# Kernel tuning notes

Measured on AMD Instinct MI355X. Metric: run time of the kernel, lower is better.

The kernel has to match this reference:

```python
import jax, jax.numpy as jnp
import numpy as np

N = 50000
E = 800000
F_IN, F_HID, F_OUT = 128, 128, 64


def setup_inputs() -> dict:
    key = jax.random.key(0)
    ks = jax.random.split(key, 8)
    x = jax.random.normal(ks[0], (N, F_IN), dtype=jnp.float32)
    attn_edge_index = jax.random.randint(ks[1], (2, E), 0, N, dtype=jnp.int64)
    attn_edge_weight = jax.random.uniform(ks[2], (E,), dtype=jnp.float32)
    # GCNConv params (glorot-ish scale); PyG lin has no bias, conv bias added after aggregation
    W1 = jax.random.normal(ks[3], (F_IN, F_HID), dtype=jnp.float32) * (1.0 / np.sqrt(F_IN))
    b1 = jnp.zeros((F_HID,), dtype=jnp.float32)
    W2 = jax.random.normal(ks[4], (F_HID, F_OUT), dtype=jnp.float32) * (1.0 / np.sqrt(F_HID))
    b2 = jnp.zeros((F_OUT,), dtype=jnp.float32)
    return {"x": x, "attn_edge_index": attn_edge_index, "attn_edge_weight": attn_edge_weight,
            "W1": W1, "b1": b1, "W2": W2, "b2": b2}


def _gcn_norm(edge_index, edge_weight, num_nodes):
    # Add self-loops with weight 1 (PyG gcn_norm default)
    loop = jnp.arange(num_nodes, dtype=edge_index.dtype)
    src = jnp.concatenate([edge_index[0], loop])
    dst = jnp.concatenate([edge_index[1], loop])
    w = jnp.concatenate([edge_weight, jnp.ones((num_nodes,), edge_weight.dtype)])
    deg = jax.ops.segment_sum(w, dst, num_segments=num_nodes)  # in-degree weighted
    dinv = jnp.where(deg > 0, jax.lax.rsqrt(deg), 0.0)
    norm = dinv[src] * w * dinv[dst]  # symmetric normalization
    return src, dst, norm


def _gcn_conv(h, src, dst, norm, W, b, num_nodes):
    h = h @ W                                   # [N, Fout] dense transform
    msg = norm[:, None] * h[src]                # [E+N, Fout] gather-multiply
    out = jax.ops.segment_sum(msg, dst, num_segments=num_nodes)  # scatter-add
    return out + b


def reference(x, attn_edge_index, attn_edge_weight, W1, b1, W2, b2):
    num_nodes = x.shape[0]
    src, dst, norm = _gcn_norm(attn_edge_index, attn_edge_weight, num_nodes)
    h = _gcn_conv(x, src, dst, norm, W1, b1, num_nodes)
    h = jax.nn.relu(h)
    # dropout(p=0.5) is identity in eval mode
    h = _gcn_conv(h, src, dst, norm, W2, b2, num_nodes)
    return h
```

## Files before the change

### kernel.cpp

```cpp
#include <hip/hip_runtime.h>
#include <hip/hip_bf16.h>

static constexpr int FIN   = 128;
static constexpr int FHID  = 128;
static constexpr int FOUTC = 64;
static constexpr int CAP   = 48;

typedef short bf16x8 __attribute__((ext_vector_type(8)));
typedef float f32x4 __attribute__((ext_vector_type(4)));

__device__ __forceinline__ float bfbits2f(unsigned short u) {
  union { unsigned i; float f; } c; c.i = ((unsigned)u) << 16; return c.f;
}
__device__ __forceinline__ float wbits2f(unsigned u) {
  union { unsigned i; float f; } c; c.i = u; return c.f;
}
__device__ __forceinline__ unsigned f2wbits(float f) {
  union { float fv; unsigned i; } c; c.fv = f; return c.i;
}
__device__ __forceinline__ void unpack_bf2(unsigned u, float& lo, float& hi) {
  union { unsigned i; float f; } a, b;
  a.i = u << 16;
  b.i = u & 0xffff0000u;
  lo = a.f; hi = b.f;
}
__device__ __forceinline__ unsigned short f2bfbits(float f) {
  union { float fv; unsigned i; } c; c.fv = f;
  unsigned i = c.i;
  unsigned r = i + 0x7FFFu + ((i >> 16) & 1u);
  if ((i & 0x7F800000u) == 0x7F800000u) r = i;
  return (unsigned short)(r >> 16);
}
__device__ __forceinline__ int ld_idx(const void* ei, int is64, long long off) {
  return is64 ? (int)((const long long*)ei)[off] : ((const int*)ei)[off];
}
__device__ __forceinline__ float ld_f(const void* p, int isbf, long long i) {
  return isbf ? bfbits2f(((const unsigned short*)p)[i]) : ((const float*)p)[i];
}

__global__ void setup_kernel(const unsigned short* __restrict__ xb,
                             const unsigned* __restrict__ eiw, int* __restrict__ flags,
                             int* __restrict__ cnt, int n) {
  int i = blockIdx.x * 256 + threadIdx.x;
  if (i < n) cnt[i] = 0;
  if (i == 0) {
    int isbf = 1;
    for (int k = 0; k < 256; ++k) {
      unsigned e = (xb[2 * k] >> 7) & 0xFFu;
      if (e >= 0xC0u) { isbf = 0; break; }
    }
    int is64 = 1;
    for (int k = 0; k < 64; ++k)
      if (eiw[2 * k + 1] != 0u) { is64 = 0; break; }
    flags[0] = isbf;
    flags[1] = is64;
  }
}

__global__ void fill_ell(const void* __restrict__ ei, const void* __restrict__ ew,
                         const int* __restrict__ flg, int* __restrict__ cnt,
                         uint2* __restrict__ ell, int E) {
  int e = blockIdx.x * 256 + threadIdx.x;
  if (e >= E) return;
  int is64 = flg[1];
  int s = ld_idx(ei, is64, e);
  int d = ld_idx(ei, is64, (long long)E + e);
  float w = ld_f(ew, flg[0], e);
  int p = atomicAdd(&cnt[d], 1);
  if (p < CAP) ell[(size_t)d * CAP + p] = make_uint2((unsigned)s, f2wbits(w));
}

__global__ void node_dinv(int* __restrict__ cnt, const uint2* __restrict__ ell,
                          float* __restrict__ dinv, int n) {
  int wid = (blockIdx.x * 256 + threadIdx.x) >> 6;
  int lane = threadIdx.x & 63;
  if (wid >= n) return;
  int c0 = cnt[wid];
  int c = c0 > CAP ? CAP : c0;
  uint2 rec = ell[(size_t)wid * CAP + (lane < CAP ? lane : CAP - 1)];
  float w = (lane < c) ? wbits2f(rec.y) : 0.f;
#pragma unroll
  for (int off = 1; off < 64; off <<= 1) w += __shfl_xor(w, off);
  if (lane == 0) {
    if (c0 > CAP) cnt[wid] = CAP;
    dinv[wid] = rsqrtf(1.f + w);
  }
}

__global__ void norm_fix(const int* __restrict__ cnt, uint2* __restrict__ ell,
                         const float* __restrict__ dinv, int n) {
  int gid = blockIdx.x * 256 + threadIdx.x;
  if (gid >= n * CAP) return;
  int node = gid / CAP;
  int slot = gid - node * CAP;
  if (slot < cnt[node]) {
    uint2 v = ell[gid];
    ((unsigned*)ell)[2 * gid + 1] = f2wbits(wbits2f(v.y) * dinv[v.x]);
  }
}

__global__ void transpose_w(const void* __restrict__ W1, const void* __restrict__ W2,
                            const int* __restrict__ flg, unsigned short* __restrict__ Wt1,
                            unsigned short* __restrict__ Wt2) {
  int i = blockIdx.x * 256 + threadIdx.x;
  int f = flg[0];
  if (i < 128 * 128) {
    int k = i >> 7, n = i & 127;
    Wt1[n * 128 + k] = f2bfbits(ld_f(W1, f, i));
  } else {
    int j = i - 128 * 128;
    int k = j >> 6, n = j & 63;
    Wt2[n * 128 + k] = f2bfbits(ld_f(W2, f, j));
  }
}

__launch_bounds__(256)
__global__ void gather_l1(const void* __restrict__ x, const int* __restrict__ flg,
                          const int* __restrict__ cnt, const uint2* __restrict__ ell,
                          const float* __restrict__ dinv, unsigned* __restrict__ agg, int n) {
  int wid = (blockIdx.x * 256 + threadIdx.x) >> 6;
  int lane = threadIdx.x & 63;
  if (wid >= n) return;
  int c = cnt[wid];
  uint2 rec = ell[(size_t)wid * CAP + (lane < CAP ? lane : CAP - 1)];
  int rsrc = (int)rec.x;
  float rw = wbits2f(rec.y);
  float a0 = 0.f, a1 = 0.f;
  float di = dinv[wid];
  float l, h;
  int iters = (c + 7) >> 3;
  if (flg[0]) {
    const unsigned* xb = (const unsigned*)x;
    for (int it = 0; it < iters; ++it) {
      int j = it * 8;
      int sa[8];
      float wa[8];
      unsigned ua[8];
#pragma unroll
      for (int t = 0; t < 8; ++t) {
        int idx = j + t;
        bool v = idx < c;
        int sl = v ? idx : 0;
        sa[t] = __shfl(rsrc, sl);
        float ww = __shfl(rw, sl);
        wa[t] = v ? ww : 0.f;
      }
#pragma unroll
      for (int t = 0; t < 8; ++t) ua[t] = xb[(size_t)sa[t] * 64 + lane];
#pragma unroll
      for (int t = 0; t < 8; ++t) {
        unpack_bf2(ua[t], l, h);
        a0 = fmaf(wa[t], l, a0);
        a1 = fmaf(wa[t], h, a1);
      }
    }
    unpack_bf2(xb[(size_t)wid * 64 + lane], l, h);
  } else {
    const float2* xf = (const float2*)x;
    for (int it = 0; it < iters; ++it) {
      int j = it * 8;
      int sa[8];
      float wa[8];
      float2 va[8];
#pragma unroll
      for (int t = 0; t < 8; ++t) {
        int idx = j + t;
        bool v = idx < c;
        int sl = v ? idx : 0;
        sa[t] = __shfl(rsrc, sl);
        float ww = __shfl(rw, sl);
        wa[t] = v ? ww : 0.f;
      }
#pragma unroll
      for (int t = 0; t < 8; ++t) va[t] = xf[(size_t)sa[t] * 64 + lane];
#pragma unroll
      for (int t = 0; t < 8; ++t) {
        a0 = fmaf(wa[t], va[t].x, a0);
        a1 = fmaf(wa[t], va[t].y, a1);
      }
    }
    float2 v = xf[(size_t)wid * 64 + lane];
    l = v.x; h = v.y;
  }
  a0 = di * a0 + di * di * l;
  a1 = di * a1 + di * di * h;
  agg[(size_t)wid * 64 + lane] = (unsigned)f2bfbits(a0) | ((unsigned)f2bfbits(a1) << 16);
}

__launch_bounds__(256)
__global__ void gather_l2(const unsigned short* __restrict__ hw2, const int* __restrict__ flg,
                          const int* __restrict__ cnt, const uint2* __restrict__ ell,
                          const float* __restrict__ dinv, const void* __restrict__ b2,
                          void* __restrict__ out, int n) {
  int wid = (blockIdx.x * 256 + threadIdx.x) >> 6;
  int lane = threadIdx.x & 63;
  if (wid >= n) return;
  int c = cnt[wid];
  uint2 rec = ell[(size_t)wid * CAP + (lane < CAP ? lane : CAP - 1)];
  int rsrc = (int)rec.x;
  float rw = wbits2f(rec.y);
  float a = 0.f;
  int iters = (c + 7) >> 3;
  for (int it = 0; it < iters; ++it) {
    int j = it * 8;
    int sa[8];
    float wa[8];
    unsigned short va[8];
#pragma unroll
    for (int t = 0; t < 8; ++t) {
      int idx = j + t;
      bool v = idx < c;
      int sl = v ? idx : 0;
      sa[t] = __shfl(rsrc, sl);
      float ww = __shfl(rw, sl);
      wa[t] = v ? ww : 0.f;
    }
#pragma unroll
    for (int t = 0; t < 8; ++t) va[t] = hw2[(size_t)sa[t] * 64 + lane];
#pragma unroll
    for (int t = 0; t < 8; ++t) a = fmaf(wa[t], bfbits2f(va[t]), a);
  }
  float di = dinv[wid];
  a = di * a + di * di * bfbits2f(hw2[(size_t)wid * 64 + lane]);
  int isbf = flg[0];
  a += ld_f(b2, isbf, lane);
  if (isbf) ((unsigned short*)out)[(size_t)wid * 64 + lane] = f2bfbits(a);
  else ((float*)out)[(size_t)wid * 64 + lane] = a;
}

__launch_bounds__(256)
__global__ void gemm12(const unsigned short* __restrict__ agg1,
                       const unsigned short* __restrict__ Wt1,
                       const unsigned short* __restrict__ Wt2,
                       const void* __restrict__ b1, const int* __restrict__ flg,
                       unsigned short* __restrict__ hw2, int M) {
  __shared__ unsigned short As[128 * 128];
  __shared__ unsigned short W1s[128 * 128];
  __shared__ unsigned short W2s[64 * 128];
  const int tid = threadIdx.x;
  const int r0 = blockIdx.x * 128;

  for (int i = tid; i < 128 * 16; i += 256) {
    int r = i >> 4, ch = i & 15;
    uint4 v = make_uint4(0u, 0u, 0u, 0u);
    if (r0 + r < M) v = *(const uint4*)(agg1 + (size_t)(r0 + r) * 128 + ch * 8);
    *(uint4*)&As[r * 128 + ((ch ^ (r & 15)) << 3)] = v;
  }
  for (int i = tid; i < 128 * 16; i += 256) {
    int r = i >> 4, ch = i & 15;
    uint4 v = *(const uint4*)(Wt1 + (size_t)r * 128 + ch * 8);
    *(uint4*)&W1s[r * 128 + ((ch ^ (r & 15)) << 3)] = v;
  }
  for (int i = tid; i < 64 * 16; i += 256) {
    int r = i >> 4, ch = i & 15;
    uint4 v = *(const uint4*)(Wt2 + (size_t)r * 128 + ch * 8);
    *(uint4*)&W2s[r * 128 + ((ch ^ (r & 15)) << 3)] = v;
  }
  __syncthreads();

  const int lane = tid & 63;
  const int wv = tid >> 6;
  const int ln15 = lane & 15;
  const int kq = lane >> 4;
  const int wbf = flg[0];

  f32x4 acc1[2][8];
#pragma unroll
  for (int mi = 0; mi < 2; ++mi)
#pragma unroll
    for (int nt = 0; nt < 8; ++nt) acc1[mi][nt] = (f32x4){0.f, 0.f, 0.f, 0.f};
#pragma unroll
  for (int kc = 0; kc < 4; ++kc) {
    int coff = (((kc * 4 + kq) ^ ln15) << 3);
    bf16x8 a0 = *(const bf16x8*)&As[((2 * wv + 0) * 16 + ln15) * 128 + coff];
    bf16x8 a1 = *(const bf16x8*)&As[((2 * wv + 1) * 16 + ln15) * 128 + coff];
#pragma unroll
    for (int nt = 0; nt < 8; ++nt) {
      bf16x8 b = *(const bf16x8*)&W1s[(nt * 16 + ln15) * 128 + coff];
      acc1[0][nt] = __builtin_amdgcn_mfma_f32_16x16x32_bf16(a0, b, acc1[0][nt], 0, 0, 0);
      acc1[1][nt] = __builtin_amdgcn_mfma_f32_16x16x32_bf16(a1, b, acc1[1][nt], 0, 0, 0);
    }
  }

#pragma unroll
  for (int nt = 0; nt < 8; ++nt) {
    int col = nt * 16 + ln15;
    float bv = ld_f(b1, wbf, col);
#pragma unroll
    for (int mi = 0; mi < 2; ++mi) {
#pragma unroll
      for (int r = 0; r < 4; ++r) {
        int row = 32 * wv + mi * 16 + kq * 4 + r;
        float o = fmaxf(acc1[mi][nt][r] + bv, 0.f);
        As[row * 128 + ((((col >> 3)) ^ (row & 15)) << 3) + (col & 7)] = f2bfbits(o);
      }
    }
  }
  __syncthreads();

  f32x4 acc2[2][4];
#pragma unroll
  for (int mi = 0; mi < 2; ++mi)
#pragma unroll
    for (int nt = 0; nt < 4; ++nt) acc2[mi][nt] = (f32x4){0.f, 0.f, 0.f, 0.f};
#pragma unroll
  for (int kc = 0; kc < 4; ++kc) {
    int coff = (((kc * 4 + kq) ^ ln15) << 3);
    bf16x8 a0 = *(const bf16x8*)&As[((2 * wv + 0) * 16 + ln15) * 128 + coff];
    bf16x8 a1 = *(const bf16x8*)&As[((2 * wv + 1) * 16 + ln15) * 128 + coff];
#pragma unroll
    for (int nt = 0; nt < 4; ++nt) {
      bf16x8 b = *(const bf16x8*)&W2s[(nt * 16 + ln15) * 128 + coff];
      acc2[0][nt] = __builtin_amdgcn_mfma_f32_16x16x32_bf16(a0, b, acc2[0][nt], 0, 0, 0);
      acc2[1][nt] = __builtin_amdgcn_mfma_f32_16x16x32_bf16(a1, b, acc2[1][nt], 0, 0, 0);
    }
  }
#pragma unroll
  for (int nt = 0; nt < 4; ++nt) {
    int col = nt * 16 + ln15;
#pragma unroll
    for (int mi = 0; mi < 2; ++mi) {
#pragma unroll
      for (int r = 0; r < 4; ++r) {
        int gr = r0 + 32 * wv + mi * 16 + kq * 4 + r;
        if (gr < M) hw2[(size_t)gr * 64 + col] = f2bfbits(acc2[mi][nt][r]);
      }
    }
  }
}

extern "C" void kernel_launch(void* const* d_in, const int* in_sizes, int n_in, void* d_out,
                              int out_size, void* d_ws, size_t ws_size, hipStream_t stream) {
  const void* x  = d_in[0];
  const void* ei = d_in[1];
  const void* ew = d_in[2];
  const void* W1 = d_in[3];
  const void* b1 = d_in[4];
  const void* W2 = d_in[5];
  const void* b2 = d_in[6];

  const int N = in_sizes[0] / FIN;
  const int E = in_sizes[1] / 2;
  const int B = 256;
  const int NB = (N + B - 1) / B;

  int* flags   = (int*)d_ws;
  int* cnt     = flags + 16;
  float* dinv  = (float*)(cnt + N);
  unsigned short* Wt1 = (unsigned short*)(dinv + N);
  unsigned short* Wt2 = Wt1 + 128 * 128;
  uint2* ell   = (uint2*)(Wt2 + 64 * 128);
  unsigned short* agg1 = (unsigned short*)(ell + (size_t)N * CAP);
  unsigned short* hw2  = agg1 + (size_t)N * FHID;

  setup_kernel<<<NB, B, 0, stream>>>((const unsigned short*)x, (const unsigned*)ei, flags, cnt, N);
  transpose_w<<<(128 * 128 + 128 * 64) / B, B, 0, stream>>>(W1, W2, flags, Wt1, Wt2);
  fill_ell<<<(E + B - 1) / B, B, 0, stream>>>(ei, ew, flags, cnt, ell, E);
  node_dinv<<<(N + 3) / 4, B, 0, stream>>>(cnt, ell, dinv, N);
  norm_fix<<<((N * CAP) + B - 1) / B, B, 0, stream>>>(cnt, ell, dinv, N);

  gather_l1<<<(N + 3) / 4, B, 0, stream>>>(x, flags, cnt, ell, dinv, (unsigned*)agg1, N);
  gemm12<<<(N + 127) / 128, B, 0, stream>>>(agg1, Wt1, Wt2, b1, flags, hw2, N);
  gather_l2<<<(N + 3) / 4, B, 0, stream>>>(hw2, flags, cnt, ell, dinv, b2, d_out, N);
}
```

Baseline: 246.1 us.

## Merge setup kernels, drop norm_fix, pad counters, vectorize gathers with wide loads

Folds the weight transpose into the setup kernel, and replaces the norm_fix pass by multiplying each edge weight by dinv[src] inside the gather kernels. Atomic counters are padded to a 64-byte stride to spread atomic contention, and fill_ell now handles two edges per thread. Both gathers switch from per-lane 4-byte/2-byte loads to 16-byte row-segment loads, with edges split across lane groups and reduced by shuffles. This reduces launch count and extra ELL traffic and widens memory transactions, but adds cross-lane reductions, more idle lanes in the epilogue and a larger counter buffer.

Result: no change. 242.8 us (-1.4%).

```diff
diff --git a/kernel.cpp b/kernel.cpp
--- a/kernel.cpp
+++ b/kernel.cpp
@@ -5,6 +5,7 @@
 static constexpr int FHID  = 128;
 static constexpr int FOUTC = 64;
 static constexpr int CAP   = 48;
+static constexpr int CSTR  = 16;
 
 typedef short bf16x8 __attribute__((ext_vector_type(8)));
 typedef float f32x4 __attribute__((ext_vector_type(4)));
@@ -39,35 +40,66 @@
 }
 
 __global__ void setup_kernel(const unsigned short* __restrict__ xb,
-                             const unsigned* __restrict__ eiw, int* __restrict__ flags,
-                             int* __restrict__ cnt, int n) {
-  int i = blockIdx.x * 256 + threadIdx.x;
-  if (i < n) cnt[i] = 0;
-  if (i == 0) {
-    int isbf = 1;
-    for (int k = 0; k < 256; ++k) {
-      unsigned e = (xb[2 * k] >> 7) & 0xFFu;
-      if (e >= 0xC0u) { isbf = 0; break; }
-    }
-    int is64 = 1;
-    for (int k = 0; k < 64; ++k)
-      if (eiw[2 * k + 1] != 0u) { is64 = 0; break; }
-    flags[0] = isbf;
-    flags[1] = is64;
+                             const unsigned* __restrict__ eiw,
+                             const void* __restrict__ W1, const void* __restrict__ W2,
+                             int* __restrict__ flags, int* __restrict__ cnt,
+                             unsigned short* __restrict__ Wt1,
+                             unsigned short* __restrict__ Wt2, int n) {
+  const int tid = threadIdx.x;
+  const int gid = blockIdx.x * 256 + tid;
+  if (gid < n) {
+    uint4 z = make_uint4(0u, 0u, 0u, 0u);
+    uint4* p = (uint4*)(cnt + (size_t)gid * CSTR);
+    p[0] = z; p[1] = z; p[2] = z; p[3] = z;
+  }
+  if (blockIdx.x < 96) {
+    __shared__ int sflags[2];
+    if (tid < 64) {
+      unsigned short xs = xb[2 * tid];
+      unsigned long long mb = __ballot(((xs >> 7) & 0xFFu) >= 0xC0u);
+      unsigned long long m2 = __ballot(eiw[2 * tid + 1] != 0u);
+      if (tid == 0) {
+        sflags[0] = (mb == 0ull);
+        sflags[1] = (m2 == 0ull);
+        if (blockIdx.x == 0) { flags[0] = sflags[0]; flags[1] = sflags[1]; }
+      }
+    }
+    __syncthreads();
+    int f = sflags[0];
+    int i = blockIdx.x * 256 + tid;
+    if (i < 128 * 128) {
+      int k = i >> 7, nn = i & 127;
+      Wt1[nn * 128 + k] = f2bfbits(ld_f(W1, f, i));
+    } else {
+      int j = i - 128 * 128;
+      int k = j >> 6, nn = j & 63;
+      Wt2[nn * 128 + k] = f2bfbits(ld_f(W2, f, j));
+    }
   }
 }
 
 __global__ void fill_ell(const void* __restrict__ ei, const void* __restrict__ ew,
                          const int* __restrict__ flg, int* __restrict__ cnt,
-                         uint2* __restrict__ ell, int E) {
-  int e = blockIdx.x * 256 + threadIdx.x;
-  if (e >= E) return;
-  int is64 = flg[1];
-  int s = ld_idx(ei, is64, e);
-  int d = ld_idx(ei, is64, (long long)E + e);
-  float w = ld_f(ew, flg[0], e);
-  int p = atomicAdd(&cnt[d], 1);
-  if (p < CAP) ell[(size_t)d * CAP + p] = make_uint2((unsigned)s, f2wbits(w));
+                         uint2* __restrict__ ell, int E, int half) {
+  int g = blockIdx.x * 256 + threadIdx.x;
+  if (g >= half) return;
+  int is64 = flg[1], isbf = flg[0];
+  int s0 = ld_idx(ei, is64, g);
+  int d0 = ld_idx(ei, is64, (long long)E + g);
+  float w0 = ld_f(ew, isbf, g);
+  int e1 = g + half;
+  bool has1 = e1 < E;
+  int s1 = 0, d1 = 0;
+  float w1 = 0.f;
+  if (has1) {
+    s1 = ld_idx(ei, is64, e1);
+    d1 = ld_idx(ei, is64, (long long)E + e1);
+    w1 = ld_f(ew, isbf, e1);
+  }
+  int p0 = atomicAdd(&cnt[(size_t)d0 * CSTR], 1);
+  int p1 = has1 ? atomicAdd(&cnt[(size_t)d1 * CSTR], 1) : CAP;
+  if (p0 < CAP) ell[(size_t)d0 * CAP + p0] = make_uint2((unsigned)s0, f2wbits(w0));
+  if (p1 < CAP) ell[(size_t)d1 * CAP + p1] = make_uint2((unsigned)s1, f2wbits(w1));
 }
 
 __global__ void node_dinv(int* __restrict__ cnt, const uint2* __restrict__ ell,
@@ -75,116 +107,123 @@
   int wid = (blockIdx.x * 256 + threadIdx.x) >> 6;
   int lane = threadIdx.x & 63;
   if (wid >= n) return;
-  int c0 = cnt[wid];
+  int c0 = cnt[(size_t)wid * CSTR];
   int c = c0 > CAP ? CAP : c0;
-  uint2 rec = ell[(size_t)wid * CAP + (lane < CAP ? lane : CAP - 1)];
-  float w = (lane < c) ? wbits2f(rec.y) : 0.f;
+  float w = 0.f;
+  if (lane < c) w = wbits2f(ell[(size_t)wid * CAP + lane].y);
 #pragma unroll
   for (int off = 1; off < 64; off <<= 1) w += __shfl_xor(w, off);
   if (lane == 0) {
-    if (c0 > CAP) cnt[wid] = CAP;
+    if (c0 > CAP) cnt[(size_t)wid * CSTR] = CAP;
     dinv[wid] = rsqrtf(1.f + w);
-  }
-}
-
-__global__ void norm_fix(const int* __restrict__ cnt, uint2* __restrict__ ell,
-                         const float* __restrict__ dinv, int n) {
-  int gid = blockIdx.x * 256 + threadIdx.x;
-  if (gid >= n * CAP) return;
-  int node = gid / CAP;
-  int slot = gid - node * CAP;
-  if (slot < cnt[node]) {
-    uint2 v = ell[gid];
-    ((unsigned*)ell)[2 * gid + 1] = f2wbits(wbits2f(v.y) * dinv[v.x]);
-  }
-}
-
-__global__ void transpose_w(const void* __restrict__ W1, const void* __restrict__ W2,
-                            const int* __restrict__ flg, unsigned short* __restrict__ Wt1,
-                            unsigned short* __restrict__ Wt2) {
-  int i = blockIdx.x * 256 + threadIdx.x;
-  int f = flg[0];
-  if (i < 128 * 128) {
-    int k = i >> 7, n = i & 127;
-    Wt1[n * 128 + k] = f2bfbits(ld_f(W1, f, i));
-  } else {
-    int j = i - 128 * 128;
-    int k = j >> 6, n = j & 63;
-    Wt2[n * 128 + k] = f2bfbits(ld_f(W2, f, j));
   }
 }
 
 __launch_bounds__(256)
 __global__ void gather_l1(const void* __restrict__ x, const int* __restrict__ flg,
                           const int* __restrict__ cnt, const uint2* __restrict__ ell,
-                          const float* __restrict__ dinv, unsigned* __restrict__ agg, int n) {
+                          const float* __restrict__ dinv, uint4* __restrict__ agg, int n) {
   int wid = (blockIdx.x * 256 + threadIdx.x) >> 6;
   int lane = threadIdx.x & 63;
   if (wid >= n) return;
-  int c = cnt[wid];
-  uint2 rec = ell[(size_t)wid * CAP + (lane < CAP ? lane : CAP - 1)];
+  int c = cnt[(size_t)wid * CSTR];
+  float di = dinv[wid];
+  uint2 rec = make_uint2(0u, 0u);
+  if (lane < c) rec = ell[(size_t)wid * CAP + lane];
   int rsrc = (int)rec.x;
-  float rw = wbits2f(rec.y);
-  float a0 = 0.f, a1 = 0.f;
-  float di = dinv[wid];
-  float l, h;
-  int iters = (c + 7) >> 3;
+  float rw = (lane < c) ? wbits2f(rec.y) * dinv[rec.x] : 0.f;
+
   if (flg[0]) {
-    const unsigned* xb = (const unsigned*)x;
+    const uint4* xv = (const uint4*)x;
+    const int fgrp = lane & 15, egrp = lane >> 4;
+    float acc[8];
+#pragma unroll
+    for (int k = 0; k < 8; ++k) acc[k] = 0.f;
+    int iters = (c + 15) >> 4;
     for (int it = 0; it < iters; ++it) {
-      int j = it * 8;
-      int sa[8];
-      float wa[8];
-      unsigned ua[8];
-#pragma unroll
-      for (int t = 0; t < 8; ++t) {
-        int idx = j + t;
-        bool v = idx < c;
-        int sl = v ? idx : 0;
-        sa[t] = __shfl(rsrc, sl);
-        float ww = __shfl(rw, sl);
-        wa[t] = v ? ww : 0.f;
+      int b = it * 16 + egrp;
+      int i0 = b, i1 = b + 4, i2 = b + 8, i3 = b + 12;
+      int s0 = __shfl(rsrc, i0), s1 = __shfl(rsrc, i1);
+      int s2 = __shfl(rsrc, i2), s3 = __shfl(rsrc, i3);
+      float w0 = __shfl(rw, i0), w1 = __shfl(rw, i1);
+      float w2 = __shfl(rw, i2), w3 = __shfl(rw, i3);
+      s0 = i0 < c ? s0 : wid; s1 = i1 < c ? s1 : wid;
+      s2 = i2 < c ? s2 : wid; s3 = i3 < c ? s3 : wid;
+      uint4 u0 = xv[(size_t)s0 * 16 + fgrp];
+      uint4 u1 = xv[(size_t)s1 * 16 + fgrp];
+      uint4 u2 = xv[(size_t)s2 * 16 + fgrp];
+      uint4 u3 = xv[(size_t)s3 * 16 + fgrp];
+      float l, h;
+      unpack_bf2(u0.x, l, h); acc[0] = fmaf(w0, l, acc[0]); acc[1] = fmaf(w0, h, acc[1]);
+      unpack_bf2(u0.y, l, h); acc[2] = fmaf(w0, l, acc[2]); acc[3] = fmaf(w0, h, acc[3]);
+      unpack_bf2(u0.z, l, h); acc[4] = fmaf(w0, l, acc[4]); acc[5] = fmaf(w0, h, acc[5]);
+      unpack_bf2(u0.w, l, h); acc[6] = fmaf(w0, l, acc[6]); acc[7] = fmaf(w0, h, acc[7]);
+      unpack_bf2(u1.x, l, h); acc[0] = fmaf(w1, l, acc[0]); acc[1] = fmaf(w1, h, acc[1]);
+      unpack_bf2(u1.y, l, h); acc[2] = fmaf(w1, l, acc[2]); acc[3] = fmaf(w1, h, acc[3]);
+      unpack_bf2(u1.z, l, h); acc[4] = fmaf(w1, l, acc[4]); acc[5] = fmaf(w1, h, acc[5]);
+      unpack_bf2(u1.w, l, h); acc[6] = fmaf(w1, l, acc[6]); acc[7] = fmaf(w1, h, acc[7]);
+      unpack_bf2(u2.x, l, h); acc[0] = fmaf(w2, l, acc[0]); acc[1] = fmaf(w2, h, acc[1]);
+      unpack_bf2(u2.y, l, h); acc[2] = fmaf(w2, l, acc[2]); acc[3] = fmaf(w2, h, acc[3]);
+      unpack_bf2(u2.z, l, h); acc[4] = fmaf(w2, l, acc[4]); acc[5] = fmaf(w2, h, acc[5]);
+      unpack_bf2(u2.w, l, h); acc[6] = fmaf(w2, l, acc[6]); acc[7] = fmaf(w2, h, acc[7]);
+      unpack_bf2(u3.x, l, h); acc[0] = fmaf(w3, l, acc[0]); acc[1] = fmaf(w3, h, acc[1]);
+      unpack_bf2(u3.y, l, h); acc[2] = fmaf(w3, l, acc[2]); acc[3] = fmaf(w3, h, acc[3]);
+      unpack_bf2(u3.z, l, h); acc[4] = fmaf(w3, l, acc[4]); acc[5] = fmaf(w3, h, acc[5]);
+      unpack_bf2(u3.w, l, h); acc[6] = fmaf(w3, l, acc[6]); acc[7] = fmaf(w3, h, acc[7]);
+    }
+#pragma unroll
+    for (int k = 0; k < 8; ++k) {
+      acc[k] += __shfl_xor(acc[k], 16);
+      acc[k] += __shfl_xor(acc[k], 32);
+    }
+    if (lane < 16) {
+      uint4 su = xv[(size_t)wid * 16 + fgrp];
+      float s0, s1, s2, s3, s4, s5, s6, s7;
+      unpack_bf2(su.x, s0, s1); unpack_bf2(su.y, s2, s3);
+      unpack_bf2(su.z, s4, s5); unpack_bf2(su.w, s6, s7);
+      float dd = di * di;
+      float o0 = di * acc[0] + dd * s0, o1 = di * acc[1] + dd * s1;
+      float o2 = di * acc[2] + dd * s2, o3 = di * acc[3] + dd * s3;
+      float o4 = di * acc[4] + dd * s4, o5 = di * acc[5] + dd * s5;
+      float o6 = di * acc[6] + dd * s6, o7 = di * acc[7] + dd * s7;
+      uint4 pk;
+      pk.x = (unsigned)f2bfbits(o0) | ((unsigned)f2bfbits(o1) << 16);
+      pk.y = (unsigned)f2bfbits(o2) | ((unsigned)f2bfbits(o3) << 16);
+      pk.z = (unsigned)f2bfbits(o4) | ((unsigned)f2bfbits(o5) << 16);
+      pk.w = (unsigned)f2bfbits(o6) | ((unsigned)f2bfbits(o7) << 16);
+      agg[(size_t)wid * 16 + fgrp] = pk;
+    }
+  } else {
+    const float4* xf = (const float4*)x;
+    const int fgrp = lane & 31, egrp = lane >> 5;
+    float acc[4] = {0.f, 0.f, 0.f, 0.f};
+    int it8 = (c + 7) >> 3;
+    for (int it = 0; it < it8; ++it) {
+      int b = it * 8 + egrp;
+#pragma unroll
+      for (int t = 0; t < 4; ++t) {
+        int idx = b + t * 2;
+        int s = __shfl(rsrc, idx);
+        float w = __shfl(rw, idx);
+        s = idx < c ? s : wid;
+        float4 v = xf[(size_t)s * 32 + fgrp];
+        acc[0] = fmaf(w, v.x, acc[0]); acc[1] = fmaf(w, v.y, acc[1]);
+        acc[2] = fmaf(w, v.z, acc[2]); acc[3] = fmaf(w, v.w, acc[3]);
       }
-#pragma unroll
-      for (int t = 0; t < 8; ++t) ua[t] = xb[(size_t)sa[t] * 64 + lane];
-#pragma unroll
-      for (int t = 0; t < 8; ++t) {
-        unpack_bf2(ua[t], l, h);
-        a0 = fmaf(wa[t], l, a0);
-        a1 = fmaf(wa[t], h, a1);
-      }
-    }
-    unpack_bf2(xb[(size_t)wid * 64 + lane], l, h);
-  } else {
-    const float2* xf = (const float2*)x;
-    for (int it = 0; it < iters; ++it) {
-      int j = it * 8;
-      int sa[8];
-      float wa[8];
-      float2 va[8];
-#pragma unroll
-      for (int t = 0; t < 8; ++t) {
-        int idx = j + t;
-        bool v = idx < c;
-        int sl = v ? idx : 0;
-        sa[t] = __shfl(rsrc, sl);
-        float ww = __shfl(rw, sl);
-        wa[t] = v ? ww : 0.f;
-      }
-#pragma unroll
-      for (int t = 0; t < 8; ++t) va[t] = xf[(size_t)sa[t] * 64 + lane];
-#pragma unroll
-      for (int t = 0; t < 8; ++t) {
-        a0 = fmaf(wa[t], va[t].x, a0);
-        a1 = fmaf(wa[t], va[t].y, a1);
-      }
-    }
-    float2 v = xf[(size_t)wid * 64 + lane];
-    l = v.x; h = v.y;
-  }
-  a0 = di * a0 + di * di * l;
-  a1 = di * a1 + di * di * h;
-  agg[(size_t)wid * 64 + lane] = (unsigned)f2bfbits(a0) | ((unsigned)f2bfbits(a1) << 16);
+    }
+#pragma unroll
+    for (int k = 0; k < 4; ++k) acc[k] += __shfl_xor(acc[k], 32);
+    if (lane < 32) {
+      float4 sv = xf[(size_t)wid * 32 + fgrp];
+      float dd = di * di;
+      float o0 = di * acc[0] + dd * sv.x, o1 = di * acc[1] + dd * sv.y;
+      float o2 = di * acc[2] + dd * sv.z, o3 = di * acc[3] + dd * sv.w;
+      uint2 pk;
+      pk.x = (unsigned)f2bfbits(o0) | ((unsigned)f2bfbits(o1) << 16);
+      pk.y = (unsigned)f2bfbits(o2) | ((unsigned)f2bfbits(o3) << 16);
+      ((uint2*)agg)[(size_t)wid * 32 + fgrp] = pk;
+    }
+  }
 }
 
 __launch_bounds__(256)
@@ -195,37 +234,70 @@
   int wid = (blockIdx.x * 256 + threadIdx.x) >> 6;
   int lane = threadIdx.x & 63;
   if (wid >= n) return;
-  int c = cnt[wid];
-  uint2 rec = ell[(size_t)wid * CAP + (lane < CAP ? lane : CAP - 1)];
+  int c = cnt[(size_t)wid * CSTR];
+  float di = dinv[wid];
+  uint2 rec = make_uint2(0u, 0u);
+  if (lane < c) rec = ell[(size_t)wid * CAP + lane];
   int rsrc = (int)rec.x;
-  float rw = wbits2f(rec.y);
-  float a = 0.f;
-  int iters = (c + 7) >> 3;
+  float rw = (lane < c) ? wbits2f(rec.y) * dinv[rec.x] : 0.f;
+
+  const uint4* hv = (const uint4*)hw2;
+  const int fgrp = lane & 7, egrp = lane >> 3;
+  float acc[8];
+#pragma unroll
+  for (int k = 0; k < 8; ++k) acc[k] = 0.f;
+  int iters = (c + 15) >> 4;
   for (int it = 0; it < iters; ++it) {
-    int j = it * 8;
-    int sa[8];
-    float wa[8];
-    unsigned short va[8];
-#pragma unroll
-    for (int t = 0; t < 8; ++t) {
-      int idx = j + t;
-      bool v = idx < c;
-      int sl = v ? idx : 0;
-      sa[t] = __shfl(rsrc, sl);
-      float ww = __shfl(rw, sl);
-      wa[t] = v ? ww : 0.f;
-    }
-#pragma unroll
-    for (int t = 0; t < 8; ++t) va[t] = hw2[(size_t)sa[t] * 64 + lane];
-#pragma unroll
-    for (int t = 0; t < 8; ++t) a = fmaf(wa[t], bfbits2f(va[t]), a);
-  }
-  float di = dinv[wid];
-  a = di * a + di * di * bfbits2f(hw2[(size_t)wid * 64 + lane]);
-  int isbf = flg[0];
-  a += ld_f(b2, isbf, lane);
-  if (isbf) ((unsigned short*)out)[(size_t)wid * 64 + lane] = f2bfbits(a);
-  else ((float*)out)[(size_t)wid * 64 + lane] = a;
+    int i0 = it * 16 + egrp, i1 = i0 + 8;
+    int s0 = __shfl(rsrc, i0), s1 = __shfl(rsrc, i1);
+    float w0 = __shfl(rw, i0), w1 = __shfl(rw, i1);
+    s0 = i0 < c ? s0 : wid;
+    s1 = i1 < c ? s1 : wid;
+    uint4 u0 = hv[(size_t)s0 * 8 + fgrp];
+    uint4 u1 = hv[(size_t)s1 * 8 + fgrp];
+    float l, h;
+    unpack_bf2(u0.x, l, h); acc[0] = fmaf(w0, l, acc[0]); acc[1] = fmaf(w0, h, acc[1]);
+    unpack_bf2(u0.y, l, h); acc[2] = fmaf(w0, l, acc[2]); acc[3] = fmaf(w0, h, acc[3]);
+    unpack_bf2(u0.z, l, h); acc[4] = fmaf(w0, l, acc[4]); acc[5] = fmaf(w0, h, acc[5]);
+    unpack_bf2(u0.w, l, h); acc[6] = fmaf(w0, l, acc[6]); acc[7] = fmaf(w0, h, acc[7]);
+    unpack_bf2(u1.x, l, h); acc[0] = fmaf(w1, l, acc[0]); acc[1] = fmaf(w1, h, acc[1]);
+    unpack_bf2(u1.y, l, h); acc[2] = fmaf(w1, l, acc[2]); acc[3] = fmaf(w1, h, acc[3]);
+    unpack_bf2(u1.z, l, h); acc[4] = fmaf(w1, l, acc[4]); acc[5] = fmaf(w1, h, acc[5]);
+    unpack_bf2(u1.w, l, h); acc[6] = fmaf(w1, l, acc[6]); acc[7] = fmaf(w1, h, acc[7]);
+  }
+#pragma unroll
+  for (int k = 0; k < 8; ++k) {
+    acc[k] += __shfl_xor(acc[k], 8);
+    acc[k] += __shfl_xor(acc[k], 16);
+    acc[k] += __shfl_xor(acc[k], 32);
+  }
+  if (lane < 8) {
+    int isbf = flg[0];
+    uint4 su = hv[(size_t)wid * 8 + fgrp];
+    float s0, s1, s2, s3, s4, s5, s6, s7;
+    unpack_bf2(su.x, s0, s1); unpack_bf2(su.y, s2, s3);
+    unpack_bf2(su.z, s4, s5); unpack_bf2(su.w, s6, s7);
+    float dd = di * di;
+    float o0 = di * acc[0] + dd * s0 + ld_f(b2, isbf, fgrp * 8 + 0);
+    float o1 = di * acc[1] + dd * s1 + ld_f(b2, isbf, fgrp * 8 + 1);
+    float o2 = di * acc[2] + dd * s2 + ld_f(b2, isbf, fgrp * 8 + 2);
+    float o3 = di * acc[3] + dd * s3 + ld_f(b2, isbf, fgrp * 8 + 3);
+    float o4 = di * acc[4] + dd * s4 + ld_f(b2, isbf, fgrp * 8 + 4);
+    float o5 = di * acc[5] + dd * s5 + ld_f(b2, isbf, fgrp * 8 + 5);
+    float o6 = di * acc[6] + dd * s6 + ld_f(b2, isbf, fgrp * 8 + 6);
+    float o7 = di * acc[7] + dd * s7 + ld_f(b2, isbf, fgrp * 8 + 7);
+    if (isbf) {
+      uint4 pk;
+      pk.x = (unsigned)f2bfbits(o0) | ((unsigned)f2bfbits(o1) << 16);
+      pk.y = (unsigned)f2bfbits(o2) | ((unsigned)f2bfbits(o3) << 16);
+      pk.z = (unsigned)f2bfbits(o4) | ((unsigned)f2bfbits(o5) << 16);
+      pk.w = (unsigned)f2bfbits(o6) | ((unsigned)f2bfbits(o7) << 16);
+      ((uint4*)out)[(size_t)wid * 8 + fgrp] = pk;
+    } else {
+      ((float4*)out)[(size_t)wid * 16 + fgrp * 2 + 0] = make_float4(o0, o1, o2, o3);
+      ((float4*)out)[(size_t)wid * 16 + fgrp * 2 + 1] = make_float4(o4, o5, o6, o7);
+    }
+  }
 }
 
 __launch_bounds__(256)
@@ -346,20 +418,19 @@
 
   int* flags   = (int*)d_ws;
   int* cnt     = flags + 16;
-  float* dinv  = (float*)(cnt + N);
+  float* dinv  = (float*)(cnt + (size_t)N * CSTR);
   unsigned short* Wt1 = (unsigned short*)(dinv + N);
   unsigned short* Wt2 = Wt1 + 128 * 128;
   uint2* ell   = (uint2*)(Wt2 + 64 * 128);
   unsigned short* agg1 = (unsigned short*)(ell + (size_t)N * CAP);
   unsigned short* hw2  = agg1 + (size_t)N * FHID;
 
-  setup_kernel<<<NB, B, 0, stream>>>((const unsigned short*)x, (const unsigned*)ei, flags, cnt, N);
-  transpose_w<<<(128 * 128 + 128 * 64) / B, B, 0, stream>>>(W1, W2, flags, Wt1, Wt2);
-  fill_ell<<<(E + B - 1) / B, B, 0, stream>>>(ei, ew, flags, cnt, ell, E);
+  const int half = (E + 1) / 2;
+  setup_kernel<<<NB, B, 0, stream>>>((const unsigned short*)x, (const unsigned*)ei, W1, W2,
+                                     flags, cnt, Wt1, Wt2, N);
+  fill_ell<<<(half + B - 1) / B, B, 0, stream>>>(ei, ew, flags, cnt, ell, E, half);
   node_dinv<<<(N + 3) / 4, B, 0, stream>>>(cnt, ell, dinv, N);
-  norm_fix<<<((N * CAP) + B - 1) / B, B, 0, stream>>>(cnt, ell, dinv, N);
-
-  gather_l1<<<(N + 3) / 4, B, 0, stream>>>(x, flags, cnt, ell, dinv, (unsigned*)agg1, N);
+  gather_l1<<<(N + 3) / 4, B, 0, stream>>>(x, flags, cnt, ell, dinv, (uint4*)agg1, N);
   gemm12<<<(N + 127) / 128, B, 0, stream>>>(agg1, Wt1, Wt2, b1, flags, hw2, N);
   gather_l2<<<(N + 3) / 4, B, 0, stream>>>(hw2, flags, cnt, ell, dinv, b2, d_out, N);
 }
```
